# Kernel optimization log

Hardware: AMD Instinct MI355X
Metric: run time of the kernel (lower is better)

The kernel has to match this reference:

```python
import jax, jax.numpy as jnp
import numpy as np

NUM_HEAD = 16
MODEL_DIM = 1024
K_DIM = MODEL_DIM // NUM_HEAD
LN_EPS = 1e-5


def setup_inputs() -> dict:
    key = jax.random.key(0)
    ks = jax.random.split(key, 9)
    B, N, D = 4, 2048, MODEL_DIM
    scale = 1.0 / np.sqrt(D)
    return {
        "q": jax.random.normal(ks[0], (B, N, D), dtype=jnp.float32),
        "k": jax.random.normal(ks[1], (B, N, D), dtype=jnp.float32),
        "v": jax.random.normal(ks[2], (B, N, D), dtype=jnp.float32),
        "Wq": jax.random.normal(ks[3], (D, D), dtype=jnp.float32) * scale,
        "Wk": jax.random.normal(ks[4], (D, D), dtype=jnp.float32) * scale,
        "Wv": jax.random.normal(ks[5], (D, D), dtype=jnp.float32) * scale,
        "Wo": jax.random.normal(ks[6], (D, D), dtype=jnp.float32) * scale,
        "gamma": jnp.ones((D,), dtype=jnp.float32),
        "beta": jnp.zeros((D,), dtype=jnp.float32),
    }


def reference(q, k, v, Wq, Wk, Wv, Wo, gamma, beta):
    B, N, D = q.shape
    H, Dh = NUM_HEAD, K_DIM
    # QKV projections (torch Linear: x @ W.T), then split heads -> [B,H,N,Dh]
    qs = (q @ Wq.T).reshape(B, N, H, Dh).transpose(0, 2, 1, 3)
    ks = (k @ Wk.T).reshape(B, N, H, Dh).transpose(0, 2, 1, 3)
    vs = (v @ Wv.T).reshape(B, N, H, Dh).transpose(0, 2, 1, 3)
    # scaled dot-product attention
    scores = jnp.einsum("bhqd,bhkd->bhqk", qs, ks) / jnp.sqrt(jnp.float32(Dh))
    probs = jax.nn.softmax(scores, axis=-1)
    attn = jnp.einsum("bhqk,bhkd->bhqd", probs, vs)
    # merge heads and output projection
    attn = attn.transpose(0, 2, 1, 3).reshape(B, N, D)
    out = attn @ Wo.T + q  # residual
    # LayerNorm
    mu = jnp.mean(out, axis=-1, keepdims=True)
    var = jnp.var(out, axis=-1, keepdims=True)
    out = (out - mu) * jax.lax.rsqrt(var + LN_EPS) * gamma + beta
    return out
```

## Files before the change

kernel.cpp:

```cpp
#include <hip/hip_runtime.h>
#include <cstdint>
#include <math.h>

typedef __bf16 bf16x8 __attribute__((ext_vector_type(8)));
typedef float f32x2 __attribute__((ext_vector_type(2)));
typedef float f32x4 __attribute__((ext_vector_type(4)));
typedef float f32x16 __attribute__((ext_vector_type(16)));
typedef int i32x2 __attribute__((ext_vector_type(2)));
typedef unsigned u32x4 __attribute__((ext_vector_type(4)));
typedef unsigned short u16;

#define B_ 4
#define N_ 2048
#define D_ 1024
#define H_ 16
#define DH_ 64
#define M_ (B_*N_)

#define QSCALE (0.125f * 1.44269504088896f)

typedef const void __attribute__((address_space(1))) gvoid;
typedef void __attribute__((address_space(3))) lvoid;

__device__ __forceinline__ void gload16(const void* g, void* l) {
  __builtin_amdgcn_global_load_lds((gvoid*)g, (lvoid*)l, 16, 0, 0);
}

__device__ __forceinline__ u16 cvt_bf(float f) {
  __bf16 h = (__bf16)f;
  return *(u16*)&h;
}

__device__ __forceinline__ unsigned cvt_pk(float lo, float hi) {
  unsigned r;
  asm("v_cvt_pk_bf16_f32 %0, %1, %2" : "=v"(r) : "v"(lo), "v"(hi));
  return r;
}

__device__ __forceinline__ i32x2 pl32swap(unsigned a, unsigned b) {
  return __builtin_amdgcn_permlane32_swap((int)a, (int)b, false, false);
}

__device__ __forceinline__ f32x2 pk_add(f32x2 a, f32x2 b) {
  f32x2 d;
  asm("v_pk_add_f32 %0, %1, %2" : "=v"(d) : "v"(a), "v"(b));
  return d;
}
__device__ __forceinline__ f32x2 pk_mul(f32x2 a, f32x2 b) {
  f32x2 d;
  asm("v_pk_mul_f32 %0, %1, %2" : "=v"(d) : "v"(a), "v"(b));
  return d;
}
__device__ __forceinline__ float m3(float a, float b, float c) {
  return fmaxf(fmaxf(a, b), c);
}

__global__ __launch_bounds__(256) void cast_all(
    const float* __restrict__ q, const float* __restrict__ k, const float* __restrict__ v,
    const float* __restrict__ wq, const float* __restrict__ wk,
    const float* __restrict__ wv, const float* __restrict__ wo,
    u16* __restrict__ oq, u16* __restrict__ ok, u16* __restrict__ ov,
    u16* __restrict__ owq, u16* __restrict__ owk, u16* __restrict__ owv, u16* __restrict__ owo) {
  const int nb = (B_*N_*D_)/4;
  const int nw = (D_*D_)/4;
  int i = blockIdx.x * 256 + threadIdx.x;
  const float* s; u16* d;
  if (i < 3*nb) {
    if (i < nb)        { s = q; d = oq; }
    else if (i < 2*nb) { s = k; d = ok; i -= nb; }
    else               { s = v; d = ov; i -= 2*nb; }
  } else {
    i -= 3*nb;
    if (i < nw)        { s = wq; d = owq; }
    else if (i < 2*nw) { s = wk; d = owk; i -= nw; }
    else if (i < 3*nw) { s = wv; d = owv; i -= 2*nw; }
    else               { s = wo; d = owo; i -= 3*nw; }
  }
  float4 x = ((const float4*)s)[i];
  ushort4 y;
  y.x = cvt_bf(x.x); y.y = cvt_bf(x.y); y.z = cvt_bf(x.z); y.w = cvt_bf(x.w);
  ((ushort4*)d)[i] = y;
}

__global__ __launch_bounds__(256) void gemm_qkv(
    const u16* __restrict__ Aq, const u16* __restrict__ Ak, const u16* __restrict__ Av,
    const u16* __restrict__ Wq, const u16* __restrict__ Wk, const u16* __restrict__ Wv,
    u16* __restrict__ Oq, u16* __restrict__ Ok, u16* __restrict__ Ov)
{
  __shared__ __align__(16) u16 As[128*64];
  __shared__ __align__(16) u16 Bs[128*64];
  const int z = blockIdx.z;
  const u16* A = (z == 0) ? Aq : (z == 1) ? Ak : Av;
  const u16* W = (z == 0) ? Wq : (z == 1) ? Wk : Wv;
  u16* obf     = (z == 0) ? Oq : (z == 1) ? Ok : Ov;
  const float oscale = (z == 0) ? QSCALE : 1.0f;

  const int t = threadIdx.x;
  const int lane = t & 63;
  const int w = t >> 6;
  const int wr = w >> 1, wc = w & 1;
  const int m0 = blockIdx.x * 128;
  const int n0 = blockIdx.y * 128;
  f32x4 acc[4][4] = {};

  const int srow = t >> 3;
  const int scb = (t & 7) ^ (srow & 7);
  const int fr = lane & 15;
  const int fg = lane >> 4;
  const int fs7 = fr & 7;

  for (int k0 = 0; k0 < 1024; k0 += 64) {
#pragma unroll
    for (int p = 0; p < 4; ++p) {
      int r = p*32 + srow;
      gload16(A + (size_t)(m0 + r)*1024 + k0 + scb*8, &As[(p*256 + t)*8]);
      gload16(W + (size_t)(n0 + r)*1024 + k0 + scb*8, &Bs[(p*256 + t)*8]);
    }
    __syncthreads();
#pragma unroll
    for (int ks = 0; ks < 2; ++ks) {
      bf16x8 af[4], bfr[4];
#pragma unroll
      for (int i = 0; i < 4; ++i) {
        int ra = wr*64 + i*16 + fr;
        af[i]  = *(const bf16x8*)&As[ra*64 + (((ks*4 + fg) ^ fs7) * 8)];
        int rb = wc*64 + i*16 + fr;
        bfr[i] = *(const bf16x8*)&Bs[rb*64 + (((ks*4 + fg) ^ fs7) * 8)];
      }
#pragma unroll
      for (int i = 0; i < 4; ++i)
#pragma unroll
        for (int j = 0; j < 4; ++j)
          acc[i][j] = __builtin_amdgcn_mfma_f32_16x16x32_bf16(af[i], bfr[j], acc[i][j], 0, 0, 0);
    }
    __syncthreads();
  }

#pragma unroll
  for (int i = 0; i < 4; ++i) {
#pragma unroll
    for (int j = 0; j < 4; ++j) {
#pragma unroll
      for (int jj = 0; jj < 4; ++jj) {
        int row = m0 + wr*64 + i*16 + fg*4 + jj;
        int col = n0 + wc*64 + j*16 + fr;
        float val = acc[i][j][jj];
        int b = row >> 11, n = row & 2047, h = col >> 6, dh = col & 63;
        if (z != 2) {
          obf[(((size_t)(b*H_ + h))*N_ + n)*DH_ + dh] = cvt_bf(val * oscale);
        } else {
          obf[(((size_t)(b*H_ + h))*DH_ + dh)*N_ + n] = cvt_bf(val);
        }
      }
    }
  }
}

__global__ __launch_bounds__(256) void gemm_out(
    const u16* __restrict__ A, const u16* __restrict__ W,
    const float* __restrict__ resid, float* __restrict__ ofp)
{
  __shared__ __align__(16) u16 As[128*64];
  __shared__ __align__(16) u16 Bs[128*64];
  const int t = threadIdx.x;
  const int lane = t & 63;
  const int w = t >> 6;
  const int wr = w >> 1, wc = w & 1;
  const int m0 = blockIdx.x * 128;
  const int n0 = blockIdx.y * 128;
  f32x4 acc[4][4] = {};

  const int srow = t >> 3;
  const int scb = (t & 7) ^ (srow & 7);
  const int fr = lane & 15;
  const int fg = lane >> 4;
  const int fs7 = fr & 7;

  for (int k0 = 0; k0 < 1024; k0 += 64) {
#pragma unroll
    for (int p = 0; p < 4; ++p) {
      int r = p*32 + srow;
      gload16(A + (size_t)(m0 + r)*1024 + k0 + scb*8, &As[(p*256 + t)*8]);
      gload16(W + (size_t)(n0 + r)*1024 + k0 + scb*8, &Bs[(p*256 + t)*8]);
    }
    __syncthreads();
#pragma unroll
    for (int ks = 0; ks < 2; ++ks) {
      bf16x8 af[4], bfr[4];
#pragma unroll
      for (int i = 0; i < 4; ++i) {
        int ra = wr*64 + i*16 + fr;
        af[i]  = *(const bf16x8*)&As[ra*64 + (((ks*4 + fg) ^ fs7) * 8)];
        int rb = wc*64 + i*16 + fr;
        bfr[i] = *(const bf16x8*)&Bs[rb*64 + (((ks*4 + fg) ^ fs7) * 8)];
      }
#pragma unroll
      for (int i = 0; i < 4; ++i)
#pragma unroll
        for (int j = 0; j < 4; ++j)
          acc[i][j] = __builtin_amdgcn_mfma_f32_16x16x32_bf16(af[i], bfr[j], acc[i][j], 0, 0, 0);
    }
    __syncthreads();
  }

#pragma unroll
  for (int i = 0; i < 4; ++i)
#pragma unroll
    for (int j = 0; j < 4; ++j)
#pragma unroll
      for (int jj = 0; jj < 4; ++jj) {
        int row = m0 + wr*64 + i*16 + fg*4 + jj;
        int col = n0 + wc*64 + j*16 + fr;
        size_t idx = (size_t)row*1024 + col;
        ofp[idx] = acc[i][j][jj] + resid[idx];
      }
}

__device__ __forceinline__ f32x2 sp2(const f32x16& S, int i) {
  f32x2 r; r.x = S[2*i]; r.y = S[2*i + 1]; return r;
}
__device__ __forceinline__ void buildP(const f32x16& S, bf16x8* pf) {
  unsigned w0 = cvt_pk(S[0], S[1]),  w1 = cvt_pk(S[2], S[3]);
  unsigned w2 = cvt_pk(S[4], S[5]),  w3 = cvt_pk(S[6], S[7]);
  i32x2 A2 = pl32swap(w0, w2), B2 = pl32swap(w1, w3);
  u32x4 f0 = { (unsigned)A2.x, (unsigned)B2.x, (unsigned)A2.y, (unsigned)B2.y };
  pf[0] = __builtin_bit_cast(bf16x8, f0);
  unsigned w4 = cvt_pk(S[8], S[9]),   w5 = cvt_pk(S[10], S[11]);
  unsigned w6 = cvt_pk(S[12], S[13]), w7 = cvt_pk(S[14], S[15]);
  i32x2 C2 = pl32swap(w4, w6), D2 = pl32swap(w5, w7);
  u32x4 f1 = { (unsigned)C2.x, (unsigned)D2.x, (unsigned)C2.y, (unsigned)D2.y };
  pf[1] = __builtin_bit_cast(bf16x8, f1);
}

__global__ __launch_bounds__(512, 2) void flash_attn(
    const u16* __restrict__ Qs, const u16* __restrict__ Ks,
    const u16* __restrict__ VTs, u16* __restrict__ ctx)
{
  __shared__ __align__(16) u16 Klds[2][128*64];
  __shared__ __align__(16) u16 Vlds[2][64*128];
  const int t = threadIdx.x;
  const int lane = t & 63;
  const int w = t >> 6;
  const int l31 = lane & 31;
  const int h = lane >> 5;
  const int bh = blockIdx.x;
  const int q0 = blockIdx.y * 256 + w * 32;
  const u16* Qbh = Qs  + (size_t)bh * N_ * DH_;
  const u16* Kbh = Ks  + (size_t)bh * N_ * DH_;
  const u16* Vbh = VTs + (size_t)bh * DH_ * N_;

  bf16x8 qf[4];
#pragma unroll
  for (int dd = 0; dd < 4; ++dd)
    qf[dd] = *(const bf16x8*)&Qbh[(size_t)(q0 + l31)*64 + dd*16 + h*8];

  float m = -1e30f;
  f32x2 lp2 = {0.f, 0.f};
  f32x16 O0 = {}, O1 = {};

  const int krow0 = t >> 3;
  const int kcb   = (t & 7) ^ ((t >> 3) & 7);
  const int vrow0 = t >> 4;
  const int vcb   = (t & 15) ^ ((t >> 4) & 7);
  const u16* ksrc = Kbh + (size_t)krow0*64 + kcb*8;
  const u16* vsrc = Vbh + (size_t)vrow0*N_ + vcb*8;

  auto stage = [&](int buf, int kv) {
#pragma unroll
    for (int p = 0; p < 2; ++p) {
      gload16(ksrc + (size_t)(kv + p*64)*64, &Klds[buf][(p*512 + t)*8]);
      gload16(vsrc + kv + (size_t)(p*32)*N_, &Vlds[buf][(p*512 + t)*8]);
    }
  };

  const int l7 = l31 & 7;

  stage(0, 0);
  __syncthreads();
  int cur = 0;

  for (int kv0 = 0; kv0 < N_; kv0 += 128) {
    if (kv0 + 128 < N_) stage(cur ^ 1, kv0 + 128);

#pragma unroll
    for (int half = 0; half < 2; ++half) {
      const int kb = half * 64;
      f32x16 S0 = {}, S1 = {};
      __builtin_amdgcn_s_setprio(1);
#pragma unroll
      for (int dd = 0; dd < 4; ++dd) {
        int cb = ((2*dd + h) ^ l7) * 8;
        bf16x8 kf0 = *(const bf16x8*)&Klds[cur][(kb + l31)*64 + cb];
        bf16x8 kf1 = *(const bf16x8*)&Klds[cur][(kb + 32 + l31)*64 + cb];
        S0 = __builtin_amdgcn_mfma_f32_32x32x16_bf16(kf0, qf[dd], S0, 0, 0, 0);
        S1 = __builtin_amdgcn_mfma_f32_32x32x16_bf16(kf1, qf[dd], S1, 0, 0, 0);
      }
      __builtin_amdgcn_s_setprio(0);

      float t0 = m3(S0[0],  S0[1],  S0[2]);
      float t1 = m3(S0[3],  S0[4],  S0[5]);
      float t2 = m3(S0[6],  S0[7],  S0[8]);
      float t3 = m3(S0[9],  S0[10], S0[11]);
      float t4 = m3(S0[12], S0[13], S0[14]);
      float t5 = m3(S0[15], S1[0],  S1[1]);
      float t6 = m3(S1[2],  S1[3],  S1[4]);
      float t7 = m3(S1[5],  S1[6],  S1[7]);
      float t8 = m3(S1[8],  S1[9],  S1[10]);
      float t9 = m3(S1[11], S1[12], S1[13]);
      float ta = fmaxf(S1[14], S1[15]);
      float u0 = m3(t0, t1, t2);
      float u1 = m3(t3, t4, t5);
      float u2 = m3(t6, t7, t8);
      float u3 = fmaxf(t9, ta);
      float pm = m3(m3(u0, u1, u2), u3, -1e30f);
      i32x2 msw = pl32swap(__float_as_uint(pm), __float_as_uint(pm));
      pm = fmaxf(__uint_as_float((unsigned)msw.x), __uint_as_float((unsigned)msw.y));

      if (!__all(pm <= m + 8.f)) {
        float mn = fmaxf(m, pm);
        float al = __builtin_amdgcn_exp2f(m - mn);
        m = mn;
        f32x2 al2; al2.x = al; al2.y = al;
        lp2 = pk_mul(lp2, al2);
#pragma unroll
        for (int r = 0; r < 8; ++r) {
          f32x2 p0 = pk_mul(sp2(O0, r), al2);
          O0[2*r] = p0.x; O0[2*r+1] = p0.y;
          f32x2 p1 = pk_mul(sp2(O1, r), al2);
          O1[2*r] = p1.x; O1[2*r+1] = p1.y;
        }
      }

      f32x2 nm2; nm2.x = -m; nm2.y = -m;
#pragma unroll
      for (int r = 0; r < 8; ++r) {
        f32x2 p0 = pk_add(sp2(S0, r), nm2);
        S0[2*r]   = __builtin_amdgcn_exp2f(p0.x);
        S0[2*r+1] = __builtin_amdgcn_exp2f(p0.y);
        f32x2 p1 = pk_add(sp2(S1, r), nm2);
        S1[2*r]   = __builtin_amdgcn_exp2f(p1.x);
        S1[2*r+1] = __builtin_amdgcn_exp2f(p1.y);
      }

      {
        f32x2 a0 = pk_add(sp2(S0,0), sp2(S0,1));
        f32x2 a1 = pk_add(sp2(S0,2), sp2(S0,3));
        f32x2 a2 = pk_add(sp2(S0,4), sp2(S0,5));
        f32x2 a3 = pk_add(sp2(S0,6), sp2(S0,7));
        f32x2 b0 = pk_add(sp2(S1,0), sp2(S1,1));
        f32x2 b1 = pk_add(sp2(S1,2), sp2(S1,3));
        f32x2 b2 = pk_add(sp2(S1,4), sp2(S1,5));
        f32x2 b3 = pk_add(sp2(S1,6), sp2(S1,7));
        a0 = pk_add(a0, a1); a2 = pk_add(a2, a3);
        b0 = pk_add(b0, b1); b2 = pk_add(b2, b3);
        a0 = pk_add(a0, a2); b0 = pk_add(b0, b2);
        lp2 = pk_add(lp2, pk_add(a0, b0));
      }

      bf16x8 pf[4];
      buildP(S0, &pf[0]);
      buildP(S1, &pf[2]);

      __builtin_amdgcn_s_setprio(1);
#pragma unroll
      for (int ks = 0; ks < 4; ++ks) {
        int cb = ((half*8 + ks*2 + h) ^ l7) * 8;
        bf16x8 vf0 = *(const bf16x8*)&Vlds[cur][l31*128 + cb];
        bf16x8 vf1 = *(const bf16x8*)&Vlds[cur][(32 + l31)*128 + cb];
        O0 = __builtin_amdgcn_mfma_f32_32x32x16_bf16(vf0, pf[ks], O0, 0, 0, 0);
        O1 = __builtin_amdgcn_mfma_f32_32x32x16_bf16(vf1, pf[ks], O1, 0, 0, 0);
      }
      __builtin_amdgcn_s_setprio(0);
    }

    __syncthreads();
    cur ^= 1;
  }

  float lps = lp2.x + lp2.y;
  i32x2 lsw = pl32swap(__float_as_uint(lps), __float_as_uint(lps));
  float ltot = __uint_as_float((unsigned)lsw.x) + __uint_as_float((unsigned)lsw.y);
  float linv = __builtin_amdgcn_rcpf(ltot);
  f32x2 li2; li2.x = linv; li2.y = linv;

  int b = bh >> 4, hh = bh & 15;
  unsigned* crow = (unsigned*)(ctx + ((size_t)b*N_ + (q0 + l31))*D_ + hh*64);
#pragma unroll
  for (int rp = 0; rp < 8; ++rp) {
    int r = rp*2;
    int d0 = (r & 3) + 8*(r >> 2) + 4*h;
    f32x2 o0 = pk_mul(sp2(O0, rp), li2);
    f32x2 o1 = pk_mul(sp2(O1, rp), li2);
    crow[d0 >> 1]        = cvt_pk(o0.x, o0.y);
    crow[(d0 + 32) >> 1] = cvt_pk(o1.x, o1.y);
  }
}

__global__ __launch_bounds__(256) void ln_fwd(float* __restrict__ io,
    const float* __restrict__ gamma, const float* __restrict__ beta)
{
  __shared__ float red[4];
  const int t = threadIdx.x;
  const int lane = t & 63, w = t >> 6;
  float4* row = (float4*)(io + (size_t)blockIdx.x * 1024);
  float4 x = row[t];
  float s = x.x + x.y + x.z + x.w;
#pragma unroll
  for (int m = 1; m < 64; m <<= 1) s += __shfl_xor(s, m);
  if (lane == 0) red[w] = s;
  __syncthreads();
  float mean = (red[0] + red[1] + red[2] + red[3]) * (1.f/1024.f);
  __syncthreads();
  float dx0 = x.x - mean, dx1 = x.y - mean, dx2 = x.z - mean, dx3 = x.w - mean;
  float sq = dx0*dx0 + dx1*dx1 + dx2*dx2 + dx3*dx3;
#pragma unroll
  for (int m = 1; m < 64; m <<= 1) sq += __shfl_xor(sq, m);
  if (lane == 0) red[w] = sq;
  __syncthreads();
  float var = (red[0] + red[1] + red[2] + red[3]) * (1.f/1024.f);
  float rstd = rsqrtf(var + 1e-5f);
  float4 g = ((const float4*)gamma)[t];
  float4 bb = ((const float4*)beta)[t];
  float4 y;
  y.x = dx0*rstd*g.x + bb.x;
  y.y = dx1*rstd*g.y + bb.y;
  y.z = dx2*rstd*g.z + bb.z;
  y.w = dx3*rstd*g.w + bb.w;
  row[t] = y;
}

extern "C" void kernel_launch(void* const* d_in, const int* in_sizes, int n_in,
                              void* d_out, int out_size, void* d_ws, size_t ws_size,
                              hipStream_t stream) {
  const float* q     = (const float*)d_in[0];
  const float* k     = (const float*)d_in[1];
  const float* v     = (const float*)d_in[2];
  const float* Wq    = (const float*)d_in[3];
  const float* Wk    = (const float*)d_in[4];
  const float* Wv    = (const float*)d_in[5];
  const float* Wo    = (const float*)d_in[6];
  const float* gamma = (const float*)d_in[7];
  const float* beta  = (const float*)d_in[8];
  float* out = (float*)d_out;

  char* ws = (char*)d_ws;
  const size_t MB = 1024*1024;
  u16* qb  = (u16*)(ws + 0*MB);
  u16* kb  = (u16*)(ws + 16*MB);
  u16* vb  = (u16*)(ws + 32*MB);
  u16* Wqb = (u16*)(ws + 48*MB);
  u16* Wkb = (u16*)(ws + 50*MB);
  u16* Wvb = (u16*)(ws + 52*MB);
  u16* Wob = (u16*)(ws + 54*MB);
  u16* Qs  = (u16*)(ws + 56*MB);
  u16* Ks  = (u16*)(ws + 72*MB);
  u16* VTs = (u16*)(ws + 88*MB);
  u16* ctx = (u16*)(ws + 0*MB);

  const int ntot4 = 3*((B_*N_*D_)/4) + 4*((D_*D_)/4);
  cast_all<<<ntot4/256, 256, 0, stream>>>(q, k, v, Wq, Wk, Wv, Wo,
                                          qb, kb, vb, Wqb, Wkb, Wvb, Wob);

  dim3 gproj(M_/128, D_/128, 3);
  gemm_qkv<<<gproj, 256, 0, stream>>>(qb, kb, vb, Wqb, Wkb, Wvb, Qs, Ks, VTs);

  flash_attn<<<dim3(B_*H_, N_/256), 512, 0, stream>>>(Qs, Ks, VTs, ctx);

  gemm_out<<<dim3(M_/128, D_/128), 256, 0, stream>>>(ctx, Wob, q, out);

  ln_fwd<<<M_, 256, 0, stream>>>(out, gamma, beta);
}
```

Baseline: 231.3 us.

## Fuse activation bf16 cast into QKV GEMM and shrink flash-attn tiles

Drops the separate fp32-to-bf16 cast of q/k/v. The QKV GEMM now loads fp32 activations directly, converts them in registers and writes swizzled bf16 into LDS, which removes a full write-and-read pass over the three activation tensors. The flash attention kernel moves from 512-thread blocks with 128-wide KV tiles to 256-thread blocks with 64-wide KV tiles, doubling the grid and allowing four blocks per CU. The row-sum reduction is also moved after the PV MFMAs. In exchange, the GEMM A-tile loads become synchronous register loads instead of direct-to-LDS loads, and attention issues more barriers per KV element.

```diff
diff --git a/kernel.cpp b/kernel.cpp
--- a/kernel.cpp
+++ b/kernel.cpp
@@ -55,27 +55,17 @@
   return fmaxf(fmaxf(a, b), c);
 }
 
-__global__ __launch_bounds__(256) void cast_all(
-    const float* __restrict__ q, const float* __restrict__ k, const float* __restrict__ v,
-    const float* __restrict__ wq, const float* __restrict__ wk,
-    const float* __restrict__ wv, const float* __restrict__ wo,
-    u16* __restrict__ oq, u16* __restrict__ ok, u16* __restrict__ ov,
-    u16* __restrict__ owq, u16* __restrict__ owk, u16* __restrict__ owv, u16* __restrict__ owo) {
-  const int nb = (B_*N_*D_)/4;
+__global__ __launch_bounds__(256) void cast_w(
+    const float* __restrict__ a, const float* __restrict__ b,
+    const float* __restrict__ c, const float* __restrict__ e,
+    u16* __restrict__ oa, u16* __restrict__ ob, u16* __restrict__ oc, u16* __restrict__ oe) {
   const int nw = (D_*D_)/4;
   int i = blockIdx.x * 256 + threadIdx.x;
   const float* s; u16* d;
-  if (i < 3*nb) {
-    if (i < nb)        { s = q; d = oq; }
-    else if (i < 2*nb) { s = k; d = ok; i -= nb; }
-    else               { s = v; d = ov; i -= 2*nb; }
-  } else {
-    i -= 3*nb;
-    if (i < nw)        { s = wq; d = owq; }
-    else if (i < 2*nw) { s = wk; d = owk; i -= nw; }
-    else if (i < 3*nw) { s = wv; d = owv; i -= 2*nw; }
-    else               { s = wo; d = owo; i -= 3*nw; }
-  }
+  if (i < nw)        { s = a; d = oa; }
+  else if (i < 2*nw) { s = b; d = ob; i -= nw; }
+  else if (i < 3*nw) { s = c; d = oc; i -= 2*nw; }
+  else               { s = e; d = oe; i -= 3*nw; }
   float4 x = ((const float4*)s)[i];
   ushort4 y;
   y.x = cvt_bf(x.x); y.y = cvt_bf(x.y); y.z = cvt_bf(x.z); y.w = cvt_bf(x.w);
@@ -83,16 +73,16 @@
 }
 
 __global__ __launch_bounds__(256) void gemm_qkv(
-    const u16* __restrict__ Aq, const u16* __restrict__ Ak, const u16* __restrict__ Av,
+    const float* __restrict__ Aq, const float* __restrict__ Ak, const float* __restrict__ Av,
     const u16* __restrict__ Wq, const u16* __restrict__ Wk, const u16* __restrict__ Wv,
     u16* __restrict__ Oq, u16* __restrict__ Ok, u16* __restrict__ Ov)
 {
   __shared__ __align__(16) u16 As[128*64];
   __shared__ __align__(16) u16 Bs[128*64];
   const int z = blockIdx.z;
-  const u16* A = (z == 0) ? Aq : (z == 1) ? Ak : Av;
-  const u16* W = (z == 0) ? Wq : (z == 1) ? Wk : Wv;
-  u16* obf     = (z == 0) ? Oq : (z == 1) ? Ok : Ov;
+  const float* A = (z == 0) ? Aq : (z == 1) ? Ak : Av;
+  const u16* W  = (z == 0) ? Wq : (z == 1) ? Wk : Wv;
+  u16* obf      = (z == 0) ? Oq : (z == 1) ? Ok : Ov;
   const float oscale = (z == 0) ? QSCALE : 1.0f;
 
   const int t = threadIdx.x;
@@ -104,17 +94,31 @@
   f32x4 acc[4][4] = {};
 
   const int srow = t >> 3;
-  const int scb = (t & 7) ^ (srow & 7);
+  const int physcb = t & 7;
+  const int wcb = physcb ^ (srow & 7);
   const int fr = lane & 15;
   const int fg = lane >> 4;
   const int fs7 = fr & 7;
 
   for (int k0 = 0; k0 < 1024; k0 += 64) {
 #pragma unroll
+    for (int p = 0; p < 4; ++p)
+      gload16(W + (size_t)(n0 + p*32 + srow)*1024 + k0 + wcb*8, &Bs[(p*256 + t)*8]);
+    float4 a0[4], a1[4];
+#pragma unroll
     for (int p = 0; p < 4; ++p) {
-      int r = p*32 + srow;
-      gload16(A + (size_t)(m0 + r)*1024 + k0 + scb*8, &As[(p*256 + t)*8]);
-      gload16(W + (size_t)(n0 + r)*1024 + k0 + scb*8, &Bs[(p*256 + t)*8]);
+      int row = p*32 + srow;
+      int lc = (physcb ^ (row & 7)) * 8;
+      const float* src = A + (size_t)(m0 + row)*1024 + k0 + lc;
+      a0[p] = *(const float4*)src;
+      a1[p] = *(const float4*)(src + 4);
+    }
+#pragma unroll
+    for (int p = 0; p < 4; ++p) {
+      int row = p*32 + srow;
+      u32x4 wv = { cvt_pk(a0[p].x, a0[p].y), cvt_pk(a0[p].z, a0[p].w),
+                   cvt_pk(a1[p].x, a1[p].y), cvt_pk(a1[p].z, a1[p].w) };
+      *(u32x4*)&As[row*64 + physcb*8] = wv;
     }
     __syncthreads();
 #pragma unroll
@@ -232,19 +236,19 @@
   pf[1] = __builtin_bit_cast(bf16x8, f1);
 }
 
-__global__ __launch_bounds__(512, 2) void flash_attn(
+__global__ __launch_bounds__(256, 4) void flash_attn(
     const u16* __restrict__ Qs, const u16* __restrict__ Ks,
     const u16* __restrict__ VTs, u16* __restrict__ ctx)
 {
-  __shared__ __align__(16) u16 Klds[2][128*64];
-  __shared__ __align__(16) u16 Vlds[2][64*128];
+  __shared__ __align__(16) u16 Klds[2][64*64];
+  __shared__ __align__(16) u16 Vlds[2][64*64];
   const int t = threadIdx.x;
   const int lane = t & 63;
   const int w = t >> 6;
   const int l31 = lane & 31;
   const int h = lane >> 5;
   const int bh = blockIdx.x;
-  const int q0 = blockIdx.y * 256 + w * 32;
+  const int q0 = blockIdx.y * 128 + w * 32;
   const u16* Qbh = Qs  + (size_t)bh * N_ * DH_;
   const u16* Kbh = Ks  + (size_t)bh * N_ * DH_;
   const u16* Vbh = VTs + (size_t)bh * DH_ * N_;
@@ -258,18 +262,16 @@
   f32x2 lp2 = {0.f, 0.f};
   f32x16 O0 = {}, O1 = {};
 
-  const int krow0 = t >> 3;
-  const int kcb   = (t & 7) ^ ((t >> 3) & 7);
-  const int vrow0 = t >> 4;
-  const int vcb   = (t & 15) ^ ((t >> 4) & 7);
-  const u16* ksrc = Kbh + (size_t)krow0*64 + kcb*8;
-  const u16* vsrc = Vbh + (size_t)vrow0*N_ + vcb*8;
+  const int srow = t >> 3;
+  const int scb  = (t & 7) ^ (srow & 7);
+  const u16* ksrc = Kbh + (size_t)srow*64 + scb*8;
+  const u16* vsrc = Vbh + (size_t)srow*N_ + scb*8;
 
   auto stage = [&](int buf, int kv) {
 #pragma unroll
     for (int p = 0; p < 2; ++p) {
-      gload16(ksrc + (size_t)(kv + p*64)*64, &Klds[buf][(p*512 + t)*8]);
-      gload16(vsrc + kv + (size_t)(p*32)*N_, &Vlds[buf][(p*512 + t)*8]);
+      gload16(ksrc + (size_t)(kv + p*32)*64, &Klds[buf][(p*256 + t)*8]);
+      gload16(vsrc + kv + (size_t)(p*32)*N_, &Vlds[buf][(p*256 + t)*8]);
     }
   };
 
@@ -279,98 +281,94 @@
   __syncthreads();
   int cur = 0;
 
-  for (int kv0 = 0; kv0 < N_; kv0 += 128) {
-    if (kv0 + 128 < N_) stage(cur ^ 1, kv0 + 128);
-
-#pragma unroll
-    for (int half = 0; half < 2; ++half) {
-      const int kb = half * 64;
-      f32x16 S0 = {}, S1 = {};
-      __builtin_amdgcn_s_setprio(1);
-#pragma unroll
-      for (int dd = 0; dd < 4; ++dd) {
-        int cb = ((2*dd + h) ^ l7) * 8;
-        bf16x8 kf0 = *(const bf16x8*)&Klds[cur][(kb + l31)*64 + cb];
-        bf16x8 kf1 = *(const bf16x8*)&Klds[cur][(kb + 32 + l31)*64 + cb];
-        S0 = __builtin_amdgcn_mfma_f32_32x32x16_bf16(kf0, qf[dd], S0, 0, 0, 0);
-        S1 = __builtin_amdgcn_mfma_f32_32x32x16_bf16(kf1, qf[dd], S1, 0, 0, 0);
+  for (int kv0 = 0; kv0 < N_; kv0 += 64) {
+    if (kv0 + 64 < N_) stage(cur ^ 1, kv0 + 64);
+
+    f32x16 S0 = {}, S1 = {};
+    __builtin_amdgcn_s_setprio(1);
+#pragma unroll
+    for (int dd = 0; dd < 4; ++dd) {
+      int cb = ((dd*2 + h) ^ l7) * 8;
+      bf16x8 kf0 = *(const bf16x8*)&Klds[cur][l31*64 + cb];
+      bf16x8 kf1 = *(const bf16x8*)&Klds[cur][(32 + l31)*64 + cb];
+      S0 = __builtin_amdgcn_mfma_f32_32x32x16_bf16(kf0, qf[dd], S0, 0, 0, 0);
+      S1 = __builtin_amdgcn_mfma_f32_32x32x16_bf16(kf1, qf[dd], S1, 0, 0, 0);
+    }
+    __builtin_amdgcn_s_setprio(0);
+
+    float t0 = m3(S0[0],  S0[1],  S0[2]);
+    float t1 = m3(S0[3],  S0[4],  S0[5]);
+    float t2 = m3(S0[6],  S0[7],  S0[8]);
+    float t3 = m3(S0[9],  S0[10], S0[11]);
+    float t4 = m3(S0[12], S0[13], S0[14]);
+    float t5 = m3(S0[15], S1[0],  S1[1]);
+    float t6 = m3(S1[2],  S1[3],  S1[4]);
+    float t7 = m3(S1[5],  S1[6],  S1[7]);
+    float t8 = m3(S1[8],  S1[9],  S1[10]);
+    float t9 = m3(S1[11], S1[12], S1[13]);
+    float ta = fmaxf(S1[14], S1[15]);
+    float u0 = m3(t0, t1, t2);
+    float u1 = m3(t3, t4, t5);
+    float u2 = m3(t6, t7, t8);
+    float u3 = fmaxf(t9, ta);
+    float pm = m3(m3(u0, u1, u2), u3, -1e30f);
+    i32x2 msw = pl32swap(__float_as_uint(pm), __float_as_uint(pm));
+    pm = fmaxf(__uint_as_float((unsigned)msw.x), __uint_as_float((unsigned)msw.y));
+
+    if (!__all(pm <= m + 8.f)) {
+      float mn = fmaxf(m, pm);
+      float al = __builtin_amdgcn_exp2f(m - mn);
+      m = mn;
+      f32x2 al2; al2.x = al; al2.y = al;
+      lp2 = pk_mul(lp2, al2);
+#pragma unroll
+      for (int r = 0; r < 8; ++r) {
+        f32x2 p0 = pk_mul(sp2(O0, r), al2);
+        O0[2*r] = p0.x; O0[2*r+1] = p0.y;
+        f32x2 p1 = pk_mul(sp2(O1, r), al2);
+        O1[2*r] = p1.x; O1[2*r+1] = p1.y;
       }
-      __builtin_amdgcn_s_setprio(0);
-
-      float t0 = m3(S0[0],  S0[1],  S0[2]);
-      float t1 = m3(S0[3],  S0[4],  S0[5]);
-      float t2 = m3(S0[6],  S0[7],  S0[8]);
-      float t3 = m3(S0[9],  S0[10], S0[11]);
-      float t4 = m3(S0[12], S0[13], S0[14]);
-      float t5 = m3(S0[15], S1[0],  S1[1]);
-      float t6 = m3(S1[2],  S1[3],  S1[4]);
-      float t7 = m3(S1[5],  S1[6],  S1[7]);
-      float t8 = m3(S1[8],  S1[9],  S1[10]);
-      float t9 = m3(S1[11], S1[12], S1[13]);
-      float ta = fmaxf(S1[14], S1[15]);
-      float u0 = m3(t0, t1, t2);
-      float u1 = m3(t3, t4, t5);
-      float u2 = m3(t6, t7, t8);
-      float u3 = fmaxf(t9, ta);
-      float pm = m3(m3(u0, u1, u2), u3, -1e30f);
-      i32x2 msw = pl32swap(__float_as_uint(pm), __float_as_uint(pm));
-      pm = fmaxf(__uint_as_float((unsigned)msw.x), __uint_as_float((unsigned)msw.y));
-
-      if (!__all(pm <= m + 8.f)) {
-        float mn = fmaxf(m, pm);
-        float al = __builtin_amdgcn_exp2f(m - mn);
-        m = mn;
-        f32x2 al2; al2.x = al; al2.y = al;
-        lp2 = pk_mul(lp2, al2);
-#pragma unroll
-        for (int r = 0; r < 8; ++r) {
-          f32x2 p0 = pk_mul(sp2(O0, r), al2);
-          O0[2*r] = p0.x; O0[2*r+1] = p0.y;
-          f32x2 p1 = pk_mul(sp2(O1, r), al2);
-          O1[2*r] = p1.x; O1[2*r+1] = p1.y;
-        }
-      }
-
-      f32x2 nm2; nm2.x = -m; nm2.y = -m;
-#pragma unroll
-      for (int r = 0; r < 8; ++r) {
-        f32x2 p0 = pk_add(sp2(S0, r), nm2);
-        S0[2*r]   = __builtin_amdgcn_exp2f(p0.x);
-        S0[2*r+1] = __builtin_amdgcn_exp2f(p0.y);
-        f32x2 p1 = pk_add(sp2(S1, r), nm2);
-        S1[2*r]   = __builtin_amdgcn_exp2f(p1.x);
-        S1[2*r+1] = __builtin_amdgcn_exp2f(p1.y);
-      }
-
-      {
-        f32x2 a0 = pk_add(sp2(S0,0), sp2(S0,1));
-        f32x2 a1 = pk_add(sp2(S0,2), sp2(S0,3));
-        f32x2 a2 = pk_add(sp2(S0,4), sp2(S0,5));
-        f32x2 a3 = pk_add(sp2(S0,6), sp2(S0,7));
-        f32x2 b0 = pk_add(sp2(S1,0), sp2(S1,1));
-        f32x2 b1 = pk_add(sp2(S1,2), sp2(S1,3));
-        f32x2 b2 = pk_add(sp2(S1,4), sp2(S1,5));
-        f32x2 b3 = pk_add(sp2(S1,6), sp2(S1,7));
-        a0 = pk_add(a0, a1); a2 = pk_add(a2, a3);
-        b0 = pk_add(b0, b1); b2 = pk_add(b2, b3);
-        a0 = pk_add(a0, a2); b0 = pk_add(b0, b2);
-        lp2 = pk_add(lp2, pk_add(a0, b0));
-      }
-
-      bf16x8 pf[4];
-      buildP(S0, &pf[0]);
-      buildP(S1, &pf[2]);
-
-      __builtin_amdgcn_s_setprio(1);
-#pragma unroll
-      for (int ks = 0; ks < 4; ++ks) {
-        int cb = ((half*8 + ks*2 + h) ^ l7) * 8;
-        bf16x8 vf0 = *(const bf16x8*)&Vlds[cur][l31*128 + cb];
-        bf16x8 vf1 = *(const bf16x8*)&Vlds[cur][(32 + l31)*128 + cb];
-        O0 = __builtin_amdgcn_mfma_f32_32x32x16_bf16(vf0, pf[ks], O0, 0, 0, 0);
-        O1 = __builtin_amdgcn_mfma_f32_32x32x16_bf16(vf1, pf[ks], O1, 0, 0, 0);
-      }
-      __builtin_amdgcn_s_setprio(0);
+    }
+
+    f32x2 nm2; nm2.x = -m; nm2.y = -m;
+#pragma unroll
+    for (int r = 0; r < 8; ++r) {
+      f32x2 p0 = pk_add(sp2(S0, r), nm2);
+      S0[2*r]   = __builtin_amdgcn_exp2f(p0.x);
+      S0[2*r+1] = __builtin_amdgcn_exp2f(p0.y);
+      f32x2 p1 = pk_add(sp2(S1, r), nm2);
+      S1[2*r]   = __builtin_amdgcn_exp2f(p1.x);
+      S1[2*r+1] = __builtin_amdgcn_exp2f(p1.y);
+    }
+
+    bf16x8 pf[4];
+    buildP(S0, &pf[0]);
+    buildP(S1, &pf[2]);
+
+    __builtin_amdgcn_s_setprio(1);
+#pragma unroll
+    for (int ks = 0; ks < 4; ++ks) {
+      int cb = ((ks*2 + h) ^ l7) * 8;
+      bf16x8 vf0 = *(const bf16x8*)&Vlds[cur][l31*64 + cb];
+      bf16x8 vf1 = *(const bf16x8*)&Vlds[cur][(32 + l31)*64 + cb];
+      O0 = __builtin_amdgcn_mfma_f32_32x32x16_bf16(vf0, pf[ks], O0, 0, 0, 0);
+      O1 = __builtin_amdgcn_mfma_f32_32x32x16_bf16(vf1, pf[ks], O1, 0, 0, 0);
+    }
+    __builtin_amdgcn_s_setprio(0);
+
+    {
+      f32x2 a0 = pk_add(sp2(S0,0), sp2(S0,1));
+      f32x2 a1 = pk_add(sp2(S0,2), sp2(S0,3));
+      f32x2 a2 = pk_add(sp2(S0,4), sp2(S0,5));
+      f32x2 a3 = pk_add(sp2(S0,6), sp2(S0,7));
+      f32x2 b0 = pk_add(sp2(S1,0), sp2(S1,1));
+      f32x2 b1 = pk_add(sp2(S1,2), sp2(S1,3));
+      f32x2 b2 = pk_add(sp2(S1,4), sp2(S1,5));
+      f32x2 b3 = pk_add(sp2(S1,6), sp2(S1,7));
+      a0 = pk_add(a0, a1); a2 = pk_add(a2, a3);
+      b0 = pk_add(b0, b1); b2 = pk_add(b2, b3);
+      a0 = pk_add(a0, a2); b0 = pk_add(b0, b2);
+      lp2 = pk_add(lp2, pk_add(a0, b0));
     }
 
     __syncthreads();
@@ -445,26 +443,22 @@
 
   char* ws = (char*)d_ws;
   const size_t MB = 1024*1024;
-  u16* qb  = (u16*)(ws + 0*MB);
-  u16* kb  = (u16*)(ws + 16*MB);
-  u16* vb  = (u16*)(ws + 32*MB);
-  u16* Wqb = (u16*)(ws + 48*MB);
-  u16* Wkb = (u16*)(ws + 50*MB);
-  u16* Wvb = (u16*)(ws + 52*MB);
-  u16* Wob = (u16*)(ws + 54*MB);
-  u16* Qs  = (u16*)(ws + 56*MB);
-  u16* Ks  = (u16*)(ws + 72*MB);
-  u16* VTs = (u16*)(ws + 88*MB);
-  u16* ctx = (u16*)(ws + 0*MB);
-
-  const int ntot4 = 3*((B_*N_*D_)/4) + 4*((D_*D_)/4);
-  cast_all<<<ntot4/256, 256, 0, stream>>>(q, k, v, Wq, Wk, Wv, Wo,
-                                          qb, kb, vb, Wqb, Wkb, Wvb, Wob);
+  u16* Wqb = (u16*)(ws + 0*MB);
+  u16* Wkb = (u16*)(ws + 2*MB);
+  u16* Wvb = (u16*)(ws + 4*MB);
+  u16* Wob = (u16*)(ws + 6*MB);
+  u16* Qs  = (u16*)(ws + 8*MB);
+  u16* Ks  = (u16*)(ws + 24*MB);
+  u16* VTs = (u16*)(ws + 40*MB);
+  u16* ctx = (u16*)(ws + 56*MB);
+
+  const int nw4 = 4*((D_*D_)/4);
+  cast_w<<<nw4/256, 256, 0, stream>>>(Wq, Wk, Wv, Wo, Wqb, Wkb, Wvb, Wob);
 
   dim3 gproj(M_/128, D_/128, 3);
-  gemm_qkv<<<gproj, 256, 0, stream>>>(qb, kb, vb, Wqb, Wkb, Wvb, Qs, Ks, VTs);
-
-  flash_attn<<<dim3(B_*H_, N_/256), 512, 0, stream>>>(Qs, Ks, VTs, ctx);
+  gemm_qkv<<<gproj, 256, 0, stream>>>(q, k, v, Wqb, Wkb, Wvb, Qs, Ks, VTs);
+
+  flash_attn<<<dim3(B_*H_, N_/128), 256, 0, stream>>>(Qs, Ks, VTs, ctx);
 
   gemm_out<<<dim3(M_/128, D_/128), 256, 0, stream>>>(ctx, Wob, q, out);
 
```

Result: no change. 233.1 us (+0.8%).
